# Performance work log

Hardware: AMD Instinct MI355X
Metric: run time of the kernel (lower is better)

Reference implementation:

```python
import jax, jax.numpy as jnp
import numpy as np

RANK = 32
W0 = 30.0


def lip_linear(x, w, c, b=None):
    # LipschitzLinear: scale rows of w so row-wise L1 norm <= softplus(c)
    scale = jnp.minimum(jax.nn.softplus(c) / jnp.sum(jnp.abs(w), axis=-1), 1.0)
    y = x @ (w * scale[:, None]).T
    return y + b if b is not None else y


def setup_inputs() -> dict:
    key = jax.random.key(0)
    ks = jax.random.split(key, 20)
    d = {}
    d['coords'] = jax.random.normal(ks[0], (8, 32768, 3), dtype=jnp.float32)
    d['latents'] = jax.random.normal(ks[1], (8, 128), dtype=jnp.float32)
    d['nf_w_first'] = jax.random.normal(ks[2], (256, 3), dtype=jnp.float32)
    d['nf_b_first'] = jax.random.normal(ks[3], (256,), dtype=jnp.float32)
    d['nf_c_first'] = jax.random.uniform(ks[4], (1,), dtype=jnp.float32)
    d['nf_w_hid'] = jax.random.normal(ks[5], (3, 256, 256), dtype=jnp.float32)
    d['nf_b_hid'] = jax.random.normal(ks[6], (3, 256), dtype=jnp.float32)
    d['nf_c_hid'] = jax.random.uniform(ks[7], (3,), dtype=jnp.float32)
    d['nf_w_last'] = jax.random.normal(ks[8], (1, 256), dtype=jnp.float32)
    d['nf_b_last'] = jax.random.normal(ks[9], (1,), dtype=jnp.float32)
    d['nf_c_last'] = jax.random.uniform(ks[10], (1,), dtype=jnp.float32)
    d['Aw_first'] = jax.random.normal(ks[11], (96, 128), dtype=jnp.float32)
    d['Ac_first'] = jax.random.uniform(ks[12], (1,), dtype=jnp.float32)
    d['Aw_hid'] = jax.random.normal(ks[13], (3, 8192, 128), dtype=jnp.float32)
    d['Ac_hid'] = jax.random.uniform(ks[14], (3,), dtype=jnp.float32)
    d['Bw'] = jax.random.normal(ks[15], (4, 8192, 128), dtype=jnp.float32)
    d['Bc'] = jax.random.uniform(ks[16], (4,), dtype=jnp.float32)
    d['hbw'] = jax.random.normal(ks[17], (4, 256, 128), dtype=jnp.float32)
    d['hbc'] = jax.random.uniform(ks[18], (4,), dtype=jnp.float32)
    return d


def reference(coords, latents, nf_w_first, nf_b_first, nf_c_first, nf_w_hid, nf_b_hid, nf_c_hid,
              nf_w_last, nf_b_last, nf_c_last, Aw_first, Ac_first, Aw_hid, Ac_hid, Bw, Bc, hbw, hbc):
    T = latents.shape[0]
    # assemble per-layer params: (nf_w, nf_b, nf_c, A_w, A_c, B_w, B_c, hb_w, hb_c)
    layers = [(nf_w_first, nf_b_first, nf_c_first, Aw_first, Ac_first, Bw[0], Bc[0], hbw[0], hbc[0])]
    for j in range(nf_w_hid.shape[0]):
        layers.append((nf_w_hid[j], nf_b_hid[j], nf_c_hid[j], Aw_hid[j], Ac_hid[j],
                       Bw[j + 1], Bc[j + 1], hbw[j + 1], hbc[j + 1]))

    x = coords  # [T, N, d_in]
    for (w, b, c, aw, ac, bw, bc, hw, hc) in layers:
        d_out, d_in = w.shape
        A = lip_linear(latents, aw, ac).reshape(T, d_in, RANK)   # [T, d_in, r]
        B = lip_linear(latents, bw, bc).reshape(T, RANK, d_out)  # [T, r, d_out]
        bias = lip_linear(latents, hw, hc)                       # [T, d_out]
        base = lip_linear(x, w, c, b)                            # [T, N, d_out]
        mod = jnp.einsum('tnr,tro->tno', jnp.einsum('tni,tir->tnr', x, A), B)
        x = jnp.sin(W0 * (base + mod + bias[:, None, :]))
    return lip_linear(x, nf_w_last, nf_c_last, nf_b_last)  # [T, N, 1]
```

## Files before the change

### kernel.cpp

```cpp
#include <hip/hip_runtime.h>
#include <math.h>

#define W0F 30.0f
#define NPTS 32768

#define C_30_OVER_2PI 4.774648292756860070
#define C_2PI         6.283185307179586477

typedef double v4d __attribute__((ext_vector_type(4)));

#define OFF_M     0ull
#define SZ_M      2097152ull
#define OFF_CB    (OFF_M + SZ_M)
#define SZ_CB     8192ull
#define OFF_AF    (OFF_CB + SZ_CB)
#define SZ_AF     262144ull
#define OFF_BF    (OFF_AF + SZ_AF)
#define SZ_BF     262144ull
#define OFF_HB    (OFF_BF + SZ_BF)
#define SZ_HB     8192ull
#define OFF_NSC   (OFF_HB + SZ_HB)
#define SZ_NSC    2048ull
#define OFF_BSWZ  (OFF_NSC + SZ_NSC)
#define SZ_BSWZ   2097152ull
#define OFF_X0    (OFF_BSWZ + SZ_BSWZ)

__global__ __launch_bounds__(256) void setup1(
    const float* __restrict__ latents,
    const float* __restrict__ AwF, const float* __restrict__ AcF,
    const float* __restrict__ AwH, const float* __restrict__ AcH,
    const float* __restrict__ Bw,  const float* __restrict__ Bc,
    const float* __restrict__ hbw, const float* __restrict__ hbc,
    const float* __restrict__ wF,  const float* __restrict__ cF,
    const float* __restrict__ wH,  const float* __restrict__ cH,
    const float* __restrict__ wL,  const float* __restrict__ cL,
    float* __restrict__ AF, float* __restrict__ BFo,
    float* __restrict__ HBo, float* __restrict__ NSC)
{
    __shared__ float lat[1024];
    int tid = threadIdx.x;
    for (int j = tid; j < 1024; j += 256) lat[j] = latents[j];
    __syncthreads();
    int g = blockIdx.x * 256 + tid;
    if (g < 58464) {
        const float* src; float c; float* dst; int stride;
        if (g < 96) {
            src = AwF + g * 128; c = AcF[0]; dst = AF + g; stride = 8192;
        } else if (g < 24672) {
            int q = g - 96; int l = 1 + q / 8192;
            src = AwH + (size_t)q * 128; c = AcH[l - 1];
            dst = AF + (size_t)l * 8 * 8192 + (q % 8192); stride = 8192;
        } else if (g < 57440) {
            int q = g - 24672; int l = q / 8192;
            src = Bw + (size_t)q * 128; c = Bc[l];
            dst = BFo + (size_t)l * 8 * 8192 + (q % 8192); stride = 8192;
        } else {
            int q = g - 57440; int l = q / 256;
            src = hbw + (size_t)q * 128; c = hbc[l];
            dst = HBo + l * 8 * 256 + (q % 256); stride = 256;
        }
        double l1 = 0.0;
        double acc[8] = {0,0,0,0,0,0,0,0};
        for (int kk = 0; kk < 32; ++kk) {
            float4 w4 = ((const float4*)src)[kk];
            l1 += fabs((double)w4.x) + fabs((double)w4.y)
                + fabs((double)w4.z) + fabs((double)w4.w);
            int k = kk * 4;
            #pragma unroll
            for (int t = 0; t < 8; ++t) {
                const float* lp = &lat[t * 128 + k];
                acc[t] = fma((double)w4.x, (double)lp[0], acc[t]);
                acc[t] = fma((double)w4.y, (double)lp[1], acc[t]);
                acc[t] = fma((double)w4.z, (double)lp[2], acc[t]);
                acc[t] = fma((double)w4.w, (double)lp[3], acc[t]);
            }
        }
        double s = fmin(log1p(exp((double)c)) / l1, 1.0);
        #pragma unroll
        for (int t = 0; t < 8; ++t) dst[(size_t)t * stride] = (float)(acc[t] * s);
    } else if (g < 59489) {
        int h = g - 58464;
        if (h < 256) {
            const float* src = wF + h * 3;
            double l1 = fabs((double)src[0]) + fabs((double)src[1]) + fabs((double)src[2]);
            NSC[h] = (float)fmin(log1p(exp((double)cF[0])) / l1, 1.0);
        } else if (h < 1024) {
            int q = h - 256; int l = 1 + q / 256;
            const float* src = wH + (size_t)q * 256;
            double l1 = 0.0;
            for (int kk = 0; kk < 64; ++kk) {
                float4 w4 = ((const float4*)src)[kk];
                l1 += fabs((double)w4.x) + fabs((double)w4.y)
                    + fabs((double)w4.z) + fabs((double)w4.w);
            }
            NSC[256 + q] = (float)fmin(log1p(exp((double)cH[l - 1])) / l1, 1.0);
        } else {
            double l1 = 0.0;
            for (int kk = 0; kk < 64; ++kk) {
                float4 w4 = ((const float4*)wL)[kk];
                l1 += fabs((double)w4.x) + fabs((double)w4.y)
                    + fabs((double)w4.z) + fabs((double)w4.w);
            }
            NSC[1024] = (float)fmin(log1p(exp((double)cL[0])) / l1, 1.0);
        }
    }
}

__global__ __launch_bounds__(256) void setup2(
    const float* __restrict__ wF, const float* __restrict__ bF,
    const float* __restrict__ wH, const float* __restrict__ bH,
    const float* __restrict__ AF, const float* __restrict__ BFi,
    const float* __restrict__ HBi, const float* __restrict__ NSC,
    float* __restrict__ Mb, float* __restrict__ CBb)
{
    int b = blockIdx.x; int t = b / 49; int rem = b % 49;
    int o = threadIdx.x;
    int l, i0, ni;
    if (rem == 0) { l = 0; i0 = 0; ni = 3; }
    else { l = 1 + (rem - 1) / 16; i0 = ((rem - 1) % 16) * 16; ni = 16; }
    size_t ltb = (size_t)(l * 8 + t);
    const float* af = AF + ltb * 8192;
    const float* bf = BFi + ltb * 8192;
    double sc = (double)NSC[l * 256 + o];
    float bcol[32];
    #pragma unroll
    for (int r = 0; r < 32; ++r) bcol[r] = bf[r * 256 + o];
    for (int ii = 0; ii < ni; ++ii) {
        int i = i0 + ii;
        float wv = (l == 0) ? wF[o * 3 + i] : wH[(size_t)((l - 1) * 256 + o) * 256 + i];
        double m = (double)wv * sc;
        #pragma unroll
        for (int r = 0; r < 32; ++r)
            m = fma((double)af[i * 32 + r], (double)bcol[r], m);
        Mb[ltb * 65536 + (size_t)i * 256 + o] = (float)m;
    }
    if (rem == 0 || ((rem - 1) % 16) == 0) {
        double bb = (l == 0) ? (double)bF[o] : (double)bH[(l - 1) * 256 + o];
        CBb[ltb * 256 + o] = (float)(bb + (double)HBi[ltb * 256 + o]);
    }
}

__global__ __launch_bounds__(256) void setup3(
    const float* __restrict__ Mb, float* __restrict__ Bswz)
{
    int gid = blockIdx.x * 256 + threadIdx.x;
    int e    = gid & 3;
    int lane = (gid >> 2) & 63;
    int h    = (gid >> 8) & 1;
    int s    = (gid >> 9) & 63;
    int ltc  = gid >> 15;
    int q = lane >> 4, c16 = lane & 15;
    int ltb = ltc >> 1, ch = ltc & 1;
    int n = h * 4 + e;
    Bswz[gid] = Mb[(size_t)ltb * 65536 + (size_t)(4 * s + q) * 256
                   + ch * 128 + n * 16 + c16];
}

__device__ __forceinline__ float sin30(double z) {
    double u = z * C_30_OVER_2PI;
    double r = u - rint(u);
    return sinf((float)(r * C_2PI));
}

__global__ __launch_bounds__(256) void layer0_k(
    const float* __restrict__ coords, const float* __restrict__ Mb,
    const float* __restrict__ CBb, float* __restrict__ X, int tbase)
{
    __shared__ float Ms[3][256];
    __shared__ float cbs[256];
    int tid = threadIdx.x;
    int tl = blockIdx.x >> 10; int rb = blockIdx.x & 1023;
    int t = tbase + tl;
    const float* Mt = Mb + (size_t)t * 65536;
    Ms[0][tid] = Mt[tid]; Ms[1][tid] = Mt[256 + tid]; Ms[2][tid] = Mt[512 + tid];
    cbs[tid] = CBb[t * 256 + tid];
    __syncthreads();
    int r = rb * 32 + (tid >> 3); int lane8 = tid & 7;
    const float* cp = coords + ((size_t)t * NPTS + r) * 3;
    double c0 = (double)cp[0], c1 = (double)cp[1], c2 = (double)cp[2];
    float* xo = X + (size_t)tl * NPTS * 256 + (size_t)(r >> 4) * 4096 + (r & 15);
#define L0E(col) sin30(fma(c2, (double)Ms[2][col], fma(c1, (double)Ms[1][col], \
                  fma(c0, (double)Ms[0][col], (double)cbs[col]))))
    #pragma unroll
    for (int j = 0; j < 8; ++j) {
        int col = 4 * lane8 + 32 * j;
        int cs  = lane8 + 8 * j;
        float* p = xo + cs * 64;
        p[0]  = L0E(col + 0);
        p[16] = L0E(col + 1);
        p[32] = L0E(col + 2);
        p[48] = L0E(col + 3);
    }
#undef L0E
}

__global__ __launch_bounds__(256, 4) void gemm_sin(
    const float* __restrict__ Xsrc, float* __restrict__ Xdst,
    const float* __restrict__ Bswz, const float* __restrict__ CBb,
    int l, int tbase, int swz_out)
{
    int tid = threadIdx.x;
    int b = blockIdx.x;
    int tl = b >> 10;
    int rb = (b >> 1) & 511;
    int ch = b & 1;
    size_t ltb = (size_t)(l * 8 + tbase + tl);
    const float* cbp = CBb + ltb * 256 + ch * 128;
    int wave = tid >> 6, lane = tid & 63;
    int q = lane >> 4, c16 = lane & 15;
    const float* ap = Xsrc + (size_t)tl * NPTS * 256 + (size_t)rb * 16384
                    + (size_t)wave * 4096 + lane;
    const float* bzl = Bswz + ((size_t)ltb * 2 + ch) * 32768 + lane * 4;
    v4d acc0 = {0.,0.,0.,0.}, acc1 = {0.,0.,0.,0.}, acc2 = {0.,0.,0.,0.},
        acc3 = {0.,0.,0.,0.}, acc4 = {0.,0.,0.,0.}, acc5 = {0.,0.,0.,0.},
        acc6 = {0.,0.,0.,0.}, acc7 = {0.,0.,0.,0.};
    float  a0 = ap[0];
    float4 b00 = *(const float4*)(bzl + 0 * 256);
    float4 b10 = *(const float4*)(bzl + 1 * 256);
    float  a1 = ap[64];
    float4 b01 = *(const float4*)(bzl + 2 * 256);
    float4 b11 = *(const float4*)(bzl + 3 * 256);
    float  a2 = ap[128];
    float4 b02 = *(const float4*)(bzl + 4 * 256);
    float4 b12 = *(const float4*)(bzl + 5 * 256);
    #pragma unroll 3
    for (int s = 0; s < 64; ++s) {
        double av = (double)a0;
#define TILE(n, bf) { acc##n = __builtin_amdgcn_mfma_f64_16x16x4f64(          \
                               av, (double)(bf), acc##n, 0, 0, 0); }
        TILE(0, b00.x) TILE(1, b00.y) TILE(2, b00.z) TILE(3, b00.w)
        TILE(4, b10.x) TILE(5, b10.y) TILE(6, b10.z) TILE(7, b10.w)
#undef TILE
        int sp = (s < 61) ? s + 3 : 63;
        a0 = a1; a1 = a2; a2 = ap[64 * sp];
        b00 = b01; b10 = b11; b01 = b02; b11 = b12;
        b02 = *(const float4*)(bzl + (size_t)(2 * sp + 0) * 256);
        b12 = *(const float4*)(bzl + (size_t)(2 * sp + 1) * 256);
    }
    v4d zz = {0., 0., 0., 0.};
    v4d p1 = __builtin_amdgcn_mfma_f64_16x16x4f64((double)(1 << c16), 1.0, zz, 0, 0, 0);
    v4d p2 = __builtin_amdgcn_mfma_f64_16x16x4f64(1.0, (double)(1 << c16), zz, 0, 0, 0);
    int r0 = 61 - __builtin_clzll((unsigned long long)p1[0]);
    int r1 = 61 - __builtin_clzll((unsigned long long)p1[1]);
    int r2 = 61 - __builtin_clzll((unsigned long long)p1[2]);
    int r3 = 61 - __builtin_clzll((unsigned long long)p1[3]);
    int c0 = 61 - __builtin_clzll((unsigned long long)p2[0]);
    int c1 = 61 - __builtin_clzll((unsigned long long)p2[1]);
    int c2 = 61 - __builtin_clzll((unsigned long long)p2[2]);
    int c3 = 61 - __builtin_clzll((unsigned long long)p2[3]);

    if (swz_out) {
        float* Xw = Xdst + (size_t)tl * NPTS * 256 + (size_t)rb * 16384
                  + (size_t)wave * 4096 + (size_t)ch * 2048;
        int o0 = (c0 >> 2) * 64 + (c0 & 3) * 16 + r0;
        int o1 = (c1 >> 2) * 64 + (c1 & 3) * 16 + r1;
        int o2 = (c2 >> 2) * 64 + (c2 & 3) * 16 + r2;
        int o3 = (c3 >> 2) * 64 + (c3 & 3) * 16 + r3;
#define EPTS(n) {                                                              \
        int cb0 = (n) * 16;                                                    \
        float* Pn = Xw + (n) * 256;                                            \
        Pn[o0] = sin30(acc##n[0] + (double)cbp[cb0 + c0]);                     \
        Pn[o1] = sin30(acc##n[1] + (double)cbp[cb0 + c1]);                     \
        Pn[o2] = sin30(acc##n[2] + (double)cbp[cb0 + c2]);                     \
        Pn[o3] = sin30(acc##n[3] + (double)cbp[cb0 + c3]); }
        EPTS(0) EPTS(1) EPTS(2) EPTS(3)
        EPTS(4) EPTS(5) EPTS(6) EPTS(7)
#undef EPTS
    } else {
        float* Xw = Xdst + ((size_t)tl * NPTS + (size_t)rb * 64) * 256
                  + ch * 128 + (size_t)(wave * 16) * 256;
#define EPT(n) {                                                               \
        int cb0 = (n) * 16;                                                    \
        Xw[r0 * 256 + cb0 + c0] = sin30(acc##n[0] + (double)cbp[cb0 + c0]);    \
        Xw[r1 * 256 + cb0 + c1] = sin30(acc##n[1] + (double)cbp[cb0 + c1]);    \
        Xw[r2 * 256 + cb0 + c2] = sin30(acc##n[2] + (double)cbp[cb0 + c2]);    \
        Xw[r3 * 256 + cb0 + c3] = sin30(acc##n[3] + (double)cbp[cb0 + c3]); }
        EPT(0) EPT(1) EPT(2) EPT(3)
        EPT(4) EPT(5) EPT(6) EPT(7)
#undef EPT
    }
}

__global__ __launch_bounds__(256) void final_k(
    const float* __restrict__ X, const float* __restrict__ wl,
    const float* __restrict__ bl, const float* __restrict__ NSC,
    float* __restrict__ out, int tbase)
{
    int tid = threadIdx.x; int w = tid >> 6; int lane = tid & 63;
    size_t row = (size_t)blockIdx.x * 4 + w;
    double ls = (double)NSC[1024];
    float4 wv = ((const float4*)wl)[lane];
    float4 xv = *(const float4*)(X + row * 256 + lane * 4);
    double d = 0.0;
    d = fma((double)wv.x, (double)xv.x, d);
    d = fma((double)wv.y, (double)xv.y, d);
    d = fma((double)wv.z, (double)xv.z, d);
    d = fma((double)wv.w, (double)xv.w, d);
    d *= ls;
    #pragma unroll
    for (int off = 32; off > 0; off >>= 1) d += __shfl_down(d, off, 64);
    if (lane == 0) out[(size_t)tbase * NPTS + row] = (float)(d + (double)bl[0]);
}

extern "C" void kernel_launch(void* const* d_in, const int* in_sizes, int n_in,
                              void* d_out, int out_size, void* d_ws, size_t ws_size,
                              hipStream_t stream)
{
    const float* coords     = (const float*)d_in[0];
    const float* latents    = (const float*)d_in[1];
    const float* nf_w_first = (const float*)d_in[2];
    const float* nf_b_first = (const float*)d_in[3];
    const float* nf_c_first = (const float*)d_in[4];
    const float* nf_w_hid   = (const float*)d_in[5];
    const float* nf_b_hid   = (const float*)d_in[6];
    const float* nf_c_hid   = (const float*)d_in[7];
    const float* nf_w_last  = (const float*)d_in[8];
    const float* nf_b_last  = (const float*)d_in[9];
    const float* nf_c_last  = (const float*)d_in[10];
    const float* Aw_first   = (const float*)d_in[11];
    const float* Ac_first   = (const float*)d_in[12];
    const float* Aw_hid     = (const float*)d_in[13];
    const float* Ac_hid     = (const float*)d_in[14];
    const float* Bw         = (const float*)d_in[15];
    const float* Bc         = (const float*)d_in[16];
    const float* hbw        = (const float*)d_in[17];
    const float* hbc        = (const float*)d_in[18];

    float* ws  = (float*)d_ws;
    float* Mb  = ws + OFF_M;
    float* CBb = ws + OFF_CB;
    float* AF  = ws + OFF_AF;
    float* BFb = ws + OFF_BF;
    float* HBb = ws + OFF_HB;
    float* NSC = ws + OFF_NSC;
    float* Bz  = ws + OFF_BSWZ;
    float* out = (float*)d_out;

    size_t availf = ws_size / sizeof(float);
    size_t xslice = (size_t)NPTS * 256;
    int T = 2;
    if (availf >= OFF_X0 + 2ull * 8 * xslice)      T = 8;
    else if (availf >= OFF_X0 + 2ull * 4 * xslice) T = 4;
    float* X0 = ws + OFF_X0;
    float* X1 = X0 + (size_t)T * xslice;

    setup1<<<233, 256, 0, stream>>>(latents, Aw_first, Ac_first, Aw_hid, Ac_hid,
                                    Bw, Bc, hbw, hbc,
                                    nf_w_first, nf_c_first, nf_w_hid, nf_c_hid,
                                    nf_w_last, nf_c_last,
                                    AF, BFb, HBb, NSC);
    setup2<<<392, 256, 0, stream>>>(nf_w_first, nf_b_first, nf_w_hid, nf_b_hid,
                                    AF, BFb, HBb, NSC, Mb, CBb);
    setup3<<<8192, 256, 0, stream>>>(Mb, Bz);
    for (int tbase = 0; tbase < 8; tbase += T) {
        layer0_k<<<1024 * T, 256, 0, stream>>>(coords, Mb, CBb, X0, tbase);
        gemm_sin<<<1024 * T, 256, 0, stream>>>(X0, X1, Bz, CBb, 1, tbase, 1);
        gemm_sin<<<1024 * T, 256, 0, stream>>>(X1, X0, Bz, CBb, 2, tbase, 1);
        gemm_sin<<<1024 * T, 256, 0, stream>>>(X0, X1, Bz, CBb, 3, tbase, 0);
        final_k<<<T * 8192, 256, 0, stream>>>(X1, nf_w_last, nf_b_last, NSC, out, tbase);
    }
}
```

Baseline: 2.260 ms.

## Run hidden-layer GEMM in place with 512-thread blocks covering both column halves

Merges the two column-half blocks into one 512-thread block, so the waves that read a row block also overwrite it after a barrier. This allows a single activation buffer instead of ping-pong buffers, which halves the workspace footprint and lets larger batch chunks (T) fit. The prefetch pipeline depth drops from three to two stages. The in-place write relies on the block-wide barrier ensuring all reads of the row slab finish before any writes. This adds sync cost and lower latency hiding in exchange for fewer launches per batch and better cache footprint.

```diff
diff --git a/kernel.cpp b/kernel.cpp
--- a/kernel.cpp
+++ b/kernel.cpp
@@ -194,49 +194,49 @@
 #undef L0E
 }
 
-__global__ __launch_bounds__(256, 4) void gemm_sin(
-    const float* __restrict__ Xsrc, float* __restrict__ Xdst,
+__global__ __launch_bounds__(512, 4) void gemm_sin(
+    float* X,
     const float* __restrict__ Bswz, const float* __restrict__ CBb,
     int l, int tbase, int swz_out)
 {
     int tid = threadIdx.x;
     int b = blockIdx.x;
-    int tl = b >> 10;
-    int rb = (b >> 1) & 511;
-    int ch = b & 1;
+    int tl = b >> 9;
+    int rb = b & 511;
     size_t ltb = (size_t)(l * 8 + tbase + tl);
-    const float* cbp = CBb + ltb * 256 + ch * 128;
     int wave = tid >> 6, lane = tid & 63;
+    int g = wave >> 1, hf = wave & 1;
     int q = lane >> 4, c16 = lane & 15;
-    const float* ap = Xsrc + (size_t)tl * NPTS * 256 + (size_t)rb * 16384
-                    + (size_t)wave * 4096 + lane;
-    const float* bzl = Bswz + ((size_t)ltb * 2 + ch) * 32768 + lane * 4;
+    const float* cbp = CBb + ltb * 256 + hf * 128;
+    const float* ap = X + (size_t)tl * NPTS * 256
+                    + (size_t)(rb * 4 + g) * 4096 + lane;
+    const float* bzl = Bswz + ((size_t)ltb * 2 + hf) * 32768 + lane * 4;
     v4d acc0 = {0.,0.,0.,0.}, acc1 = {0.,0.,0.,0.}, acc2 = {0.,0.,0.,0.},
         acc3 = {0.,0.,0.,0.}, acc4 = {0.,0.,0.,0.}, acc5 = {0.,0.,0.,0.},
         acc6 = {0.,0.,0.,0.}, acc7 = {0.,0.,0.,0.};
-    float  a0 = ap[0];
-    float4 b00 = *(const float4*)(bzl + 0 * 256);
-    float4 b10 = *(const float4*)(bzl + 1 * 256);
-    float  a1 = ap[64];
-    float4 b01 = *(const float4*)(bzl + 2 * 256);
-    float4 b11 = *(const float4*)(bzl + 3 * 256);
-    float  a2 = ap[128];
-    float4 b02 = *(const float4*)(bzl + 4 * 256);
-    float4 b12 = *(const float4*)(bzl + 5 * 256);
-    #pragma unroll 3
+    float  aC  = ap[0];
+    float4 bC0 = *(const float4*)(bzl + 0 * 256);
+    float4 bC1 = *(const float4*)(bzl + 1 * 256);
+    float  aN  = ap[64];
+    float4 bN0 = *(const float4*)(bzl + 2 * 256);
+    float4 bN1 = *(const float4*)(bzl + 3 * 256);
+    #pragma unroll 2
     for (int s = 0; s < 64; ++s) {
-        double av = (double)a0;
+        int s2 = (s < 62) ? s + 2 : 63;
+        float  aNN  = ap[64 * s2];
+        float4 bNN0 = *(const float4*)(bzl + (size_t)(s2 * 2 + 0) * 256);
+        float4 bNN1 = *(const float4*)(bzl + (size_t)(s2 * 2 + 1) * 256);
+        double av = (double)aC;
 #define TILE(n, bf) { acc##n = __builtin_amdgcn_mfma_f64_16x16x4f64(          \
                                av, (double)(bf), acc##n, 0, 0, 0); }
-        TILE(0, b00.x) TILE(1, b00.y) TILE(2, b00.z) TILE(3, b00.w)
-        TILE(4, b10.x) TILE(5, b10.y) TILE(6, b10.z) TILE(7, b10.w)
+        TILE(0, bC0.x) TILE(1, bC0.y) TILE(2, bC0.z) TILE(3, bC0.w)
+        TILE(4, bC1.x) TILE(5, bC1.y) TILE(6, bC1.z) TILE(7, bC1.w)
 #undef TILE
-        int sp = (s < 61) ? s + 3 : 63;
-        a0 = a1; a1 = a2; a2 = ap[64 * sp];
-        b00 = b01; b10 = b11; b01 = b02; b11 = b12;
-        b02 = *(const float4*)(bzl + (size_t)(2 * sp + 0) * 256);
-        b12 = *(const float4*)(bzl + (size_t)(2 * sp + 1) * 256);
-    }
+        aC = aN;  aN = aNN;
+        bC0 = bN0; bC1 = bN1; bN0 = bNN0; bN1 = bNN1;
+    }
+    __syncthreads();
+
     v4d zz = {0., 0., 0., 0.};
     v4d p1 = __builtin_amdgcn_mfma_f64_16x16x4f64((double)(1 << c16), 1.0, zz, 0, 0, 0);
     v4d p2 = __builtin_amdgcn_mfma_f64_16x16x4f64(1.0, (double)(1 << c16), zz, 0, 0, 0);
@@ -250,8 +250,8 @@
     int c3 = 61 - __builtin_clzll((unsigned long long)p2[3]);
 
     if (swz_out) {
-        float* Xw = Xdst + (size_t)tl * NPTS * 256 + (size_t)rb * 16384
-                  + (size_t)wave * 4096 + (size_t)ch * 2048;
+        float* Xw = X + (size_t)tl * NPTS * 256
+                  + (size_t)(rb * 4 + g) * 4096 + (size_t)hf * 2048;
         int o0 = (c0 >> 2) * 64 + (c0 & 3) * 16 + r0;
         int o1 = (c1 >> 2) * 64 + (c1 & 3) * 16 + r1;
         int o2 = (c2 >> 2) * 64 + (c2 & 3) * 16 + r2;
@@ -267,8 +267,8 @@
         EPTS(4) EPTS(5) EPTS(6) EPTS(7)
 #undef EPTS
     } else {
-        float* Xw = Xdst + ((size_t)tl * NPTS + (size_t)rb * 64) * 256
-                  + ch * 128 + (size_t)(wave * 16) * 256;
+        float* Xw = X + ((size_t)tl * NPTS + (size_t)(rb * 64 + g * 16)) * 256
+                  + hf * 128;
 #define EPT(n) {                                                               \
         int cb0 = (n) * 16;                                                    \
         Xw[r0 * 256 + cb0 + c0] = sin30(acc##n[0] + (double)cbp[cb0 + c0]);    \
@@ -339,10 +339,9 @@
     size_t availf = ws_size / sizeof(float);
     size_t xslice = (size_t)NPTS * 256;
     int T = 2;
-    if (availf >= OFF_X0 + 2ull * 8 * xslice)      T = 8;
-    else if (availf >= OFF_X0 + 2ull * 4 * xslice) T = 4;
+    if (availf >= OFF_X0 + 8ull * xslice)      T = 8;
+    else if (availf >= OFF_X0 + 4ull * xslice) T = 4;
     float* X0 = ws + OFF_X0;
-    float* X1 = X0 + (size_t)T * xslice;
 
     setup1<<<233, 256, 0, stream>>>(latents, Aw_first, Ac_first, Aw_hid, Ac_hid,
                                     Bw, Bc, hbw, hbc,
@@ -354,9 +353,9 @@
     setup3<<<8192, 256, 0, stream>>>(Mb, Bz);
     for (int tbase = 0; tbase < 8; tbase += T) {
         layer0_k<<<1024 * T, 256, 0, stream>>>(coords, Mb, CBb, X0, tbase);
-        gemm_sin<<<1024 * T, 256, 0, stream>>>(X0, X1, Bz, CBb, 1, tbase, 1);
-        gemm_sin<<<1024 * T, 256, 0, stream>>>(X1, X0, Bz, CBb, 2, tbase, 1);
-        gemm_sin<<<1024 * T, 256, 0, stream>>>(X0, X1, Bz, CBb, 3, tbase, 0);
-        final_k<<<T * 8192, 256, 0, stream>>>(X1, nf_w_last, nf_b_last, NSC, out, tbase);
-    }
-}
+        gemm_sin<<<512 * T, 512, 0, stream>>>(X0, Bz, CBb, 1, tbase, 1);
+        gemm_sin<<<512 * T, 512, 0, stream>>>(X0, Bz, CBb, 2, tbase, 1);
+        gemm_sin<<<512 * T, 512, 0, stream>>>(X0, Bz, CBb, 3, tbase, 0);
+        final_k<<<T * 8192, 256, 0, stream>>>(X0, nf_w_last, nf_b_last, NSC, out, tbase);
+    }
+}
```

Result: faster. 2.098 ms (-7.2%).
